# Optimization experiments

Hardware: AMD Instinct MI355X
Metric: run time of the kernel (lower is better)

Reference implementation:

```python
import jax, jax.numpy as jnp
import numpy as np

PI = np.pi
EPS_A = 1e-4


def _frft_1d(x, a):
    """Chirp-z shear FRFT along the last axis. x: complex (..., N), a: scalar order."""
    a = jnp.clip(a, EPS_A, 2.0 - EPS_A)
    N = x.shape[-1]
    x = jnp.fft.ifftshift(x, axes=-1)
    alpha = a * PI / 2.0
    tan_a2 = jnp.tan(a * PI / 4.0)
    sin_a = jnp.sin(alpha)
    n = (jnp.arange(N, dtype=jnp.float32) - (N // 2))  # [-N/2, N/2)
    c1 = jnp.exp(-1j * PI * (n ** 2) * tan_a2 / N)      # chirp (depends on a)
    c2 = jnp.exp(-1j * PI * (n ** 2) / (N * sin_a))     # kernel chirp
    y = jnp.fft.ifft(jnp.fft.fft(x * c1, axis=-1) * c2, axis=-1)
    y = y * c1 / jnp.sqrt(jnp.abs(sin_a) + 1e-12)
    return jnp.fft.fftshift(y, axes=-1)


def _frft2d(x, ax, ay):
    # width pass (last axis) with ay, then height pass with ax -- same math as the
    # per-row / per-column torch loops, fully batched.
    y = _frft_1d(x, ay)                                   # over W
    y = jnp.swapaxes(_frft_1d(jnp.swapaxes(y, -1, -2), ax), -1, -2)  # over H
    return y


def setup_inputs() -> dict:
    key = jax.random.key(0)
    kx, = jax.random.split(key, 1)
    B, C, H, W = 4, 32, 256, 256
    x = jax.random.normal(kx, (B, C, H, W), dtype=jnp.float32)
    alpha = jnp.float32(0.5)
    # 1x1 conv weight (C, 2C): module init = copy of magnitude channels
    w = jnp.zeros((C, 2 * C), dtype=jnp.float32)
    w = w.at[jnp.arange(C), jnp.arange(C)].set(1.0)
    return {"x": x, "alpha": alpha, "w": w}


def reference(x, alpha, w):
    Xc = x.astype(jnp.complex64)
    Y = _frft2d(Xc, alpha, alpha)                        # (B, C, H, W) complex
    out = jnp.concatenate([jnp.abs(Y), jnp.angle(Y) / PI], axis=1)  # (B, 2C, H, W)
    out = jnp.einsum('oc,bchw->bohw', w, out)            # 1x1 conv, no bias
    return out.astype(x.dtype)
```

## Files before the change

### kernel.cpp

```cpp
#include <hip/hip_runtime.h>
#include <math.h>

#define B_N 4
#define C_N 32
#define H_N 256
#define W_N 256
#define PI_D 3.14159265358979323846
#define LSQ 257
#define LDW 260

typedef _Float16 half8 __attribute__((ext_vector_type(8)));
typedef float f32x4 __attribute__((ext_vector_type(4)));

union H2U { unsigned int u; struct { _Float16 lo, hi; } f; };

__device__ __forceinline__ float2 cmul(float2 a, float2 b) {
    return make_float2(a.x * b.x - a.y * b.y, a.x * b.y + a.y * b.x);
}
__device__ __forceinline__ float2 f2add(float2 a, float2 b) {
    return make_float2(a.x + b.x, a.y + b.y);
}
__device__ __forceinline__ float2 f2sub(float2 a, float2 b) {
    return make_float2(a.x - b.x, a.y - b.y);
}

__device__ __forceinline__ void make_tables(int tid, const float* __restrict__ alpha_p,
                                            float2* c1l, float2* c2l, float2* twl,
                                            float* sscl) {
    if (tid < 256) {
        int j = tid;
        float a = fminf(fmaxf(alpha_p[0], 1e-4f), 2.0f - 1e-4f);
        float tan_a2 = tanf(a * (float)(PI_D / 4.0));
        float sin_a  = sinf(a * (float)(PI_D / 2.0));
        float n = (float)(j - 128);
        float n2f = n * n;
        float sn, cs;

        float u1 = n2f * tan_a2 * (1.0f / 256.0f);
        u1 -= 2.0f * floorf(u1 * 0.5f);
        __sincosf(-(float)PI_D * u1, &sn, &cs);
        c1l[j] = make_float2(cs, sn);

        float u2 = n2f / (256.0f * sin_a);
        u2 -= 2.0f * floorf(u2 * 0.5f);
        __sincosf(-(float)PI_D * u2, &sn, &cs);
        c2l[j] = make_float2(cs, sn);

        int k1 = j >> 4, t = j & 15;
        __sincosf(-(float)(2.0 * PI_D / 256.0) * (float)(t * k1), &sn, &cs);
        twl[j] = make_float2(cs, sn);

        if (j == 0) *sscl = 1.0f / sqrtf(sin_a + 1e-12f);
    }
}

template <bool INV>
__device__ __forceinline__ void fft16(float2* v) {
    const float C1 = 0.9238795325112867f, S1 = 0.3826834323650898f;
    const float C2 = 0.7071067811865476f;
    const float2 tw1 = make_float2(C1, INV ? S1 : -S1);
    const float2 tw2 = make_float2(C2, INV ? C2 : -C2);
    const float2 tw3 = make_float2(S1, INV ? C1 : -C1);
    const float2 tw4 = make_float2(0.0f, INV ? 1.0f : -1.0f);
    const float2 tw6 = make_float2(-C2, INV ? C2 : -C2);
    const float2 tw9 = make_float2(-C1, INV ? -S1 : S1);
    float2 u[16];
    #pragma unroll
    for (int n2 = 0; n2 < 4; ++n2) {
        float2 e0 = v[n2], e1 = v[4 + n2], e2 = v[8 + n2], e3 = v[12 + n2];
        float2 t0 = f2add(e0, e2), t1 = f2sub(e0, e2);
        float2 t2 = f2add(e1, e3), t3 = f2sub(e1, e3);
        float2 A0 = f2add(t0, t2);
        float2 A2 = f2sub(t0, t2);
        float2 A1, A3;
        if (!INV) { A1 = make_float2(t1.x + t3.y, t1.y - t3.x);
                    A3 = make_float2(t1.x - t3.y, t1.y + t3.x); }
        else      { A1 = make_float2(t1.x - t3.y, t1.y + t3.x);
                    A3 = make_float2(t1.x + t3.y, t1.y - t3.x); }
        u[n2] = A0;
        if (n2 == 0) { u[4 + n2] = A1;            u[8 + n2] = A2;            u[12 + n2] = A3; }
        if (n2 == 1) { u[4 + n2] = cmul(A1, tw1); u[8 + n2] = cmul(A2, tw2); u[12 + n2] = cmul(A3, tw3); }
        if (n2 == 2) { u[4 + n2] = cmul(A1, tw2); u[8 + n2] = cmul(A2, tw4); u[12 + n2] = cmul(A3, tw6); }
        if (n2 == 3) { u[4 + n2] = cmul(A1, tw3); u[8 + n2] = cmul(A2, tw6); u[12 + n2] = cmul(A3, tw9); }
    }
    #pragma unroll
    for (int k1 = 0; k1 < 4; ++k1) {
        float2 e0 = u[4 * k1], e1 = u[4 * k1 + 1], e2 = u[4 * k1 + 2], e3 = u[4 * k1 + 3];
        float2 t0 = f2add(e0, e2), t1 = f2sub(e0, e2);
        float2 t2 = f2add(e1, e3), t3 = f2sub(e1, e3);
        v[4 * k1 + 0] = f2add(t0, t2);
        v[4 * k1 + 2] = f2sub(t0, t2);
        if (!INV) { v[4 * k1 + 1] = make_float2(t1.x + t3.y, t1.y - t3.x);
                    v[4 * k1 + 3] = make_float2(t1.x - t3.y, t1.y + t3.x); }
        else      { v[4 * k1 + 1] = make_float2(t1.x - t3.y, t1.y + t3.x);
                    v[4 * k1 + 3] = make_float2(t1.x + t3.y, t1.y - t3.x); }
    }
}
#define REG(k) (4 * ((k) & 3) + ((k) >> 2))

__device__ __forceinline__ void frft_core16(float2* v, float2* __restrict__ sp,
                                            int t,
                                            const float2* __restrict__ c2l,
                                            const float2* __restrict__ twl) {
    fft16<false>(v);
    float2 w[16];
    #pragma unroll
    for (int k1 = 0; k1 < 16; ++k1)
        w[k1] = cmul(v[REG(k1)], twl[16 * k1 + t]);
    #pragma unroll
    for (int k1 = 0; k1 < 16; ++k1)
        sp[16 * k1 + (t ^ k1)] = w[k1];
    __syncthreads();
    #pragma unroll
    for (int n2 = 0; n2 < 16; ++n2)
        v[n2] = sp[16 * t + (n2 ^ t)];
    fft16<false>(v);
    #pragma unroll
    for (int k2 = 0; k2 < 16; ++k2)
        w[k2] = cmul(v[REG(k2)], c2l[t + 16 * k2]);
    fft16<true>(w);
    __syncthreads();
    #pragma unroll
    for (int m2 = 0; m2 < 16; ++m2) {
        float2 tw = twl[16 * m2 + t];
        tw.y = -tw.y;
        sp[16 * m2 + (t ^ m2)] = cmul(w[REG(m2)], tw);
    }
    __syncthreads();
    #pragma unroll
    for (int k1 = 0; k1 < 16; ++k1)
        v[k1] = sp[16 * t + (k1 ^ t)];
    fft16<true>(v);
}

__global__ __launch_bounds__(512, 4) void frft_cols_real(
        const float* __restrict__ x,
        const float* __restrict__ alpha_p,
        unsigned int* __restrict__ Yh) {
    __shared__ float2 s[32 * LSQ];
    __shared__ float2 c1l[256], c2l[256], twl[256];
    __shared__ float sscl;
    int tid = threadIdx.x;

    int blk = blockIdx.x;
    int w0 = (blk & 7) << 5;
    long long bc = blk >> 3;
    const float* xb = x + (bc << 16) + w0;

    float4 xv[4];
    #pragma unroll
    for (int p = 0; p < 4; ++p) {
        int idx = tid + (p << 9);
        int row = idx >> 3, c4 = idx & 7;
        xv[p] = *(const float4*)(xb + row * W_N + (c4 << 2));
    }

    make_tables(tid, alpha_p, c1l, c2l, twl, &sscl);

    float* fs = (float*)s;
    #pragma unroll
    for (int p = 0; p < 4; ++p) {
        int idx = tid + (p << 9);
        int row = idx >> 3, c4 = idx & 7;
        fs[(4 * c4 + 0) * (2 * LSQ) + row] = xv[p].x;
        fs[(4 * c4 + 1) * (2 * LSQ) + row] = xv[p].y;
        fs[(4 * c4 + 2) * (2 * LSQ) + row] = xv[p].z;
        fs[(4 * c4 + 3) * (2 * LSQ) + row] = xv[p].w;
    }
    __syncthreads();

    int seq = tid & 31, t = tid >> 5;
    float xs[16];
    #pragma unroll
    for (int n1 = 0; n1 < 16; ++n1)
        xs[n1] = fs[seq * (2 * LSQ) + 16 * (n1 ^ 8) + t];
    float scl_v = sscl;
    __syncthreads();

    float2 v[16];
    #pragma unroll
    for (int n1 = 0; n1 < 16; ++n1) {
        float2 c = c1l[16 * n1 + t];
        v[n1] = make_float2(xs[n1] * c.x, xs[n1] * c.y);
    }

    frft_core16(v, s + seq * LSQ, t, c2l, twl);

    float sc = scl_v * (1.0f / 256.0f);
    unsigned int* Yb = Yh + (bc << 16) + w0 + seq;
    #pragma unroll
    for (int m1 = 0; m1 < 16; ++m1) {
        float2 o = cmul(v[REG(m1)], c1l[16 * m1 + t]);
        H2U pu;
        pu.f.lo = (_Float16)(o.x * sc);
        pu.f.hi = (_Float16)(o.y * sc);
        Yb[(16 * (m1 ^ 8) + t) * W_N] = pu.u;
    }
}

__device__ __forceinline__ float fast_atan2(float y, float x) {
    float ax = fabsf(x), ay = fabsf(y);
    float mx = fmaxf(ax, ay), mn = fminf(ax, ay);
    float z = mn * __builtin_amdgcn_rcpf(fmaxf(mx, 1e-37f));
    float z2 = z * z;
    float p = fmaf(z2, -0.01172120f, 0.05265332f);
    p = fmaf(z2, p, -0.11643287f);
    p = fmaf(z2, p, 0.19354346f);
    p = fmaf(z2, p, -0.33262347f);
    p = fmaf(z2, p, 0.99997726f);
    p = p * z;
    float r = (ay > ax) ? (1.5707963f - p) : p;
    r = (x < 0.0f) ? (3.14159265f - r) : r;
    return copysignf(r, y);
}

__global__ __launch_bounds__(512, 4) void frft_rows_conv(
        const unsigned int* __restrict__ Yh,
        const float* __restrict__ alpha_p,
        const float* __restrict__ wmat, float* __restrict__ out) {
    __shared__ float2 s[32 * LSQ];
    __shared__ float2 c1l[256], c2l[256], twl[256];
    __shared__ float sscl;
    int tid = threadIdx.x;
    int t = tid & 15, ch = tid >> 4;

    int b = blockIdx.x >> 8, h = blockIdx.x & 255;
    const unsigned int* xr = Yh + (((long long)(b * C_N + ch)) << 16) + (h << 8);

    float2 v[16];
    #pragma unroll
    for (int n1 = 0; n1 < 16; ++n1) {
        H2U pu; pu.u = xr[16 * (n1 ^ 8) + t];
        v[n1] = make_float2((float)pu.f.lo, (float)pu.f.hi);
    }

    make_tables(tid, alpha_p, c1l, c2l, twl, &sscl);
    __syncthreads();

    #pragma unroll
    for (int n1 = 0; n1 < 16; ++n1)
        v[n1] = cmul(v[n1], c1l[16 * n1 + t]);

    float2* sp = s + ch * LSQ;
    frft_core16(v, sp, t, c2l, twl);

    float sc = sscl * (1.0f / 256.0f);
    #pragma unroll
    for (int m1 = 0; m1 < 16; ++m1) {
        float2 o = cmul(v[REG(m1)], c1l[16 * m1 + t]);
        float mg = sc * sqrtf(fmaf(o.x, o.x, o.y * o.y));
        float an = fast_atan2(o.y, o.x) * 0.31830988618f;
        sp[16 * (m1 ^ 8) + t] = make_float2(mg, an);
    }
    __syncthreads();

    int lane = tid & 63, wv = tid >> 6;
    int q = lane >> 4, l15 = lane & 15;

    half8 bf[2][2];
    #pragma unroll
    for (int nt = 0; nt < 2; ++nt)
        #pragma unroll
        for (int kt = 0; kt < 2; ++kt) {
            const float* wp = wmat + (nt * 16 + l15) * 64 + kt * 32 + q * 8;
            float4 wa = *(const float4*)wp;
            float4 wb = *(const float4*)(wp + 4);
            bf[nt][kt][0] = (_Float16)wa.x; bf[nt][kt][1] = (_Float16)wa.y;
            bf[nt][kt][2] = (_Float16)wa.z; bf[nt][kt][3] = (_Float16)wa.w;
            bf[nt][kt][4] = (_Float16)wb.x; bf[nt][kt][5] = (_Float16)wb.y;
            bf[nt][kt][6] = (_Float16)wb.z; bf[nt][kt][7] = (_Float16)wb.w;
        }

    f32x4 acc[2][2];
    #pragma unroll
    for (int i = 0; i < 2; ++i)
        #pragma unroll
        for (int j = 0; j < 2; ++j)
            acc[i][j] = (f32x4){0.0f, 0.0f, 0.0f, 0.0f};

    #pragma unroll
    for (int mt2 = 0; mt2 < 2; ++mt2) {
        int mt = wv * 2 + mt2;
        int w = mt * 16 + l15;
        half8 am, aa;
        #pragma unroll
        for (int j = 0; j < 8; ++j) {
            float2 fv = s[(q * 8 + j) * LSQ + w];
            am[j] = (_Float16)fv.x;
            aa[j] = (_Float16)fv.y;
        }
        #pragma unroll
        for (int nt = 0; nt < 2; ++nt) {
            acc[mt2][nt] = __builtin_amdgcn_mfma_f32_16x16x32_f16(am, bf[nt][0], acc[mt2][nt], 0, 0, 0);
            acc[mt2][nt] = __builtin_amdgcn_mfma_f32_16x16x32_f16(aa, bf[nt][1], acc[mt2][nt], 0, 0, 0);
        }
    }
    __syncthreads();

    float* Ob = (float*)s;
    #pragma unroll
    for (int mt2 = 0; mt2 < 2; ++mt2) {
        int mt = wv * 2 + mt2;
        #pragma unroll
        for (int nt = 0; nt < 2; ++nt) {
            int o = nt * 16 + l15;
            *(f32x4*)&Ob[o * LDW + mt * 16 + q * 4] = acc[mt2][nt];
        }
    }
    __syncthreads();

    int o2 = tid >> 4, i16 = tid & 15;
    float* ob = out + (((long long)(b * C_N + o2)) << 16) + (h << 8);
    #pragma unroll
    for (int p = 0; p < 4; ++p) {
        int w4 = i16 * 4 + (p << 6);
        f32x4 val = *(f32x4*)&Ob[o2 * LDW + w4];
        *(f32x4*)(ob + w4) = val;
    }
}

extern "C" void kernel_launch(void* const* d_in, const int* in_sizes, int n_in,
                              void* d_out, int out_size, void* d_ws, size_t ws_size,
                              hipStream_t stream) {
    const float* x     = (const float*)d_in[0];
    const float* alpha = (const float*)d_in[1];
    const float* wmat  = (const float*)d_in[2];
    float* out = (float*)d_out;

    unsigned int* Yh = (unsigned int*)d_ws;

    frft_cols_real<<<B_N * C_N * (W_N / 32), 512, 0, stream>>>(x, alpha, Yh);

    frft_rows_conv<<<B_N * H_N, 512, 0, stream>>>(Yh, alpha, wmat, out);
}
```

Before: 125.6 us.

## Shrink row-kernel LDS via two-phase transpose and packed fp16 feature staging

The row FRFT kernel now does its in-FFT transposes in two halves through a small per-channel scratch (18-float2 stride, 146 per channel) instead of a full 257-entry buffer. The magnitude/phase features are packed to fp16 pairs and stored channel-contiguous so the MFMA operand fetch uses 128-bit LDS reads. Together these cut LDS use enough to raise launch bounds occupancy from 4 to 6 blocks per CU, and the global loads are issued before table construction to hide their latency. The costs are extra LDS round trips with explicit waitcnt fences in the transpose, earlier rounding of features to fp16, and higher register pressure under the tighter occupancy target.

```diff
diff --git a/kernel.cpp b/kernel.cpp
--- a/kernel.cpp
+++ b/kernel.cpp
@@ -7,7 +7,10 @@
 #define W_N 256
 #define PI_D 3.14159265358979323846
 #define LSQ 257
-#define LDW 260
+#define CR   18
+#define SEQS 146
+#define FTS  36
+#define LDW  260
 
 typedef _Float16 half8 __attribute__((ext_vector_type(8)));
 typedef float f32x4 __attribute__((ext_vector_type(4)));
@@ -133,6 +136,63 @@
     fft16<true>(v);
 }
 
+#define LDS_FENCE() do {                                    \
+    asm volatile("s_waitcnt lgkmcnt(0)" ::: "memory");      \
+    __builtin_amdgcn_sched_barrier(0);                      \
+} while (0)
+
+__device__ __forceinline__ void lds_read_row16(const float2* __restrict__ rp, float2* v) {
+    #pragma unroll
+    for (int c = 0; c < 8; ++c) {
+        f32x4 r = *(const f32x4*)(rp + 2 * c);
+        v[2 * c]     = make_float2(r.x, r.y);
+        v[2 * c + 1] = make_float2(r.z, r.w);
+    }
+}
+
+__device__ __forceinline__ void xpose16(const float2* a, float2* o,
+                                        float2* __restrict__ sp, int t) {
+    bool lo = (t & 8) == 0;
+    float2* rp = sp + CR * (t & 7);
+    #pragma unroll
+    for (int r = 0; r < 8; ++r) sp[CR * r + t] = a[r];
+    LDS_FENCE();
+    if (lo) lds_read_row16(rp, o);
+    LDS_FENCE();
+    #pragma unroll
+    for (int r = 0; r < 8; ++r) sp[CR * r + t] = a[8 + r];
+    LDS_FENCE();
+    if (!lo) lds_read_row16(rp, o);
+    LDS_FENCE();
+}
+
+__device__ __forceinline__ void frft_core16_pp(float2* v, float2* __restrict__ sp,
+                                               int t,
+                                               const float2* __restrict__ c2l,
+                                               const float2* __restrict__ twl) {
+    fft16<false>(v);
+    float2 w[16];
+    #pragma unroll
+    for (int k1 = 0; k1 < 16; ++k1)
+        w[k1] = cmul(v[REG(k1)], twl[16 * k1 + t]);
+    xpose16(w, v, sp, t);
+    fft16<false>(v);
+    #pragma unroll
+    for (int k2 = 0; k2 < 16; ++k2)
+        w[k2] = cmul(v[REG(k2)], c2l[t + 16 * k2]);
+    fft16<true>(w);
+    #pragma unroll
+    for (int m2 = 0; m2 < 16; ++m2) {
+        float2 tw = twl[16 * m2 + t];
+        tw.y = -tw.y;
+        v[m2] = cmul(w[REG(m2)], tw);
+    }
+    xpose16(v, w, sp, t);
+    fft16<true>(w);
+    #pragma unroll
+    for (int i = 0; i < 16; ++i) v[i] = w[i];
+}
+
 __global__ __launch_bounds__(512, 4) void frft_cols_real(
         const float* __restrict__ x,
         const float* __restrict__ alpha_p,
@@ -214,11 +274,11 @@
     return copysignf(r, y);
 }
 
-__global__ __launch_bounds__(512, 4) void frft_rows_conv(
+__global__ __launch_bounds__(512, 6) void frft_rows_conv(
         const unsigned int* __restrict__ Yh,
         const float* __restrict__ alpha_p,
         const float* __restrict__ wmat, float* __restrict__ out) {
-    __shared__ float2 s[32 * LSQ];
+    __shared__ float2 s[32 * SEQS];
     __shared__ float2 c1l[256], c2l[256], twl[256];
     __shared__ float sscl;
     int tid = threadIdx.x;
@@ -227,31 +287,40 @@
     int b = blockIdx.x >> 8, h = blockIdx.x & 255;
     const unsigned int* xr = Yh + (((long long)(b * C_N + ch)) << 16) + (h << 8);
 
+    unsigned int u0[16];
+    #pragma unroll
+    for (int n1 = 0; n1 < 16; ++n1)
+        u0[n1] = xr[16 * (n1 ^ 8) + t];
+
+    make_tables(tid, alpha_p, c1l, c2l, twl, &sscl);
+    __syncthreads();
+
     float2 v[16];
     #pragma unroll
     for (int n1 = 0; n1 < 16; ++n1) {
-        H2U pu; pu.u = xr[16 * (n1 ^ 8) + t];
-        v[n1] = make_float2((float)pu.f.lo, (float)pu.f.hi);
-    }
-
-    make_tables(tid, alpha_p, c1l, c2l, twl, &sscl);
-    __syncthreads();
-
-    #pragma unroll
-    for (int n1 = 0; n1 < 16; ++n1)
-        v[n1] = cmul(v[n1], c1l[16 * n1 + t]);
-
-    float2* sp = s + ch * LSQ;
-    frft_core16(v, sp, t, c2l, twl);
+        H2U pu; pu.u = u0[n1];
+        float2 y = make_float2((float)pu.f.lo, (float)pu.f.hi);
+        v[n1] = cmul(y, c1l[16 * n1 + t]);
+    }
+
+    frft_core16_pp(v, s + ch * SEQS, t, c2l, twl);
 
     float sc = sscl * (1.0f / 256.0f);
+    unsigned int pk[16];
     #pragma unroll
     for (int m1 = 0; m1 < 16; ++m1) {
         float2 o = cmul(v[REG(m1)], c1l[16 * m1 + t]);
         float mg = sc * sqrtf(fmaf(o.x, o.x, o.y * o.y));
         float an = fast_atan2(o.y, o.x) * 0.31830988618f;
-        sp[16 * (m1 ^ 8) + t] = make_float2(mg, an);
-    }
+        H2U pu; pu.f.lo = (_Float16)mg; pu.f.hi = (_Float16)an;
+        pk[m1] = pu.u;
+    }
+    __syncthreads();
+
+    unsigned int* feat = (unsigned int*)s;
+    #pragma unroll
+    for (int m1 = 0; m1 < 16; ++m1)
+        feat[(16 * (m1 ^ 8) + t) * FTS + ch] = pk[m1];
     __syncthreads();
 
     int lane = tid & 63, wv = tid >> 6;
@@ -282,12 +351,16 @@
     for (int mt2 = 0; mt2 < 2; ++mt2) {
         int mt = wv * 2 + mt2;
         int w = mt * 16 + l15;
+        const uint4* fp = (const uint4*)(feat + w * FTS + q * 8);
+        uint4 ca = fp[0], cb = fp[1];
         half8 am, aa;
         #pragma unroll
         for (int j = 0; j < 8; ++j) {
-            float2 fv = s[(q * 8 + j) * LSQ + w];
-            am[j] = (_Float16)fv.x;
-            aa[j] = (_Float16)fv.y;
+            H2U pu;
+            pu.u = (j < 4) ? ((const unsigned int*)&ca)[j]
+                           : ((const unsigned int*)&cb)[j - 4];
+            am[j] = pu.f.lo;
+            aa[j] = pu.f.hi;
         }
         #pragma unroll
         for (int nt = 0; nt < 2; ++nt) {
```

After: 137.4 us. 1.09x slower.
